# Kernel tuning notes

Hardware: AMD Instinct MI355X
Metric: run time of the kernel (lower is better)

Reference implementation:

```python
import jax, jax.numpy as jnp
import numpy as np

N_NODES = 100000
N_EDGES = 3200000
IN_FEAT = 256
OUT_FEAT = 128

def setup_inputs() -> dict:
    key = jax.random.key(0)
    k1, k2, k3, k4, k5 = jax.random.split(key, 5)
    feat = jax.random.normal(k1, (N_NODES, IN_FEAT), dtype=jnp.float32)
    edge_row = jnp.sort(jax.random.randint(k2, (N_EDGES,), 0, N_NODES, dtype=jnp.int32))
    edge_col = jax.random.randint(k3, (N_EDGES,), 0, N_NODES, dtype=jnp.int32)
    edge_val = jax.random.uniform(k4, (N_EDGES,), dtype=jnp.float32)
    # Xavier-uniform init like the torch module
    limit = float(np.sqrt(6.0 / (IN_FEAT + OUT_FEAT)))
    weight = jax.random.uniform(k5, (IN_FEAT, OUT_FEAT), dtype=jnp.float32, minval=-limit, maxval=limit)
    return {"feat": feat, "edge_row": edge_row, "edge_col": edge_col, "edge_val": edge_val, "weight": weight}

def reference(feat, edge_row, edge_col, edge_val, weight):
    # feat_embedding = feat @ W            [N, out_feat]
    feat_embedding = jnp.matmul(feat, weight)
    # x = spmm(adj, feat_embedding): out[i] = sum_{edges e: row[e]=i} val[e] * femb[col[e]]
    messages = edge_val[:, None] * feat_embedding[edge_col]  # [E, out_feat]
    x = jax.ops.segment_sum(messages, edge_row, num_segments=N_NODES)
    return (feat_embedding, x)
```

## Files before the change

kernel.cpp:

```cpp
#include <hip/hip_runtime.h>
#include <hip/hip_fp16.h>

#define IN_FEAT 256
#define OUT_FEAT 128

typedef _Float16 half8 __attribute__((ext_vector_type(8)));
typedef float    f32x4 __attribute__((ext_vector_type(4)));

#define GBM 128
#define GT  512

__global__ __launch_bounds__(GT, 1) void gemm_mfma_kernel(
    const float* __restrict__ A, const float* __restrict__ W,
    float* __restrict__ C, __half* __restrict__ Ch, int M, int writeHalf)
{
    __shared__ _Float16 sA[GBM * IN_FEAT];
    __shared__ _Float16 sW[OUT_FEAT * IN_FEAT];

    const int t    = threadIdx.x;
    const int row0 = blockIdx.x * GBM;

    {
        const int row = t >> 2;
        const int kq  = t & 3;
        int grow = row0 + row; if (grow >= M) grow = M - 1;
        const float* Ap = &A[(size_t)grow * IN_FEAT];
        #pragma unroll
        for (int i = 0; i < 8; ++i) {
            int k = kq * 8 + i * 32;
            float4 a0 = *(const float4*)(Ap + k);
            float4 a1 = *(const float4*)(Ap + k + 4);
            half8 h;
            h[0]=(_Float16)a0.x; h[1]=(_Float16)a0.y; h[2]=(_Float16)a0.z; h[3]=(_Float16)a0.w;
            h[4]=(_Float16)a1.x; h[5]=(_Float16)a1.y; h[6]=(_Float16)a1.z; h[7]=(_Float16)a1.w;
            int byte = row * 512 + k * 2;
            byte ^= (row & 7) << 4;
            *(half8*)((char*)sA + byte) = h;
        }
    }
    {
        const int col = t & 127;
        const int kq  = t >> 7;
        #pragma unroll
        for (int i = 0; i < 16; ++i) {
            int k = kq * 64 + i * 4;
            _Float16 h[4];
            h[0] = (_Float16)W[(size_t)(k+0) * OUT_FEAT + col];
            h[1] = (_Float16)W[(size_t)(k+1) * OUT_FEAT + col];
            h[2] = (_Float16)W[(size_t)(k+2) * OUT_FEAT + col];
            h[3] = (_Float16)W[(size_t)(k+3) * OUT_FEAT + col];
            int byte = col * 512 + k * 2;
            byte ^= (col & 7) << 4;
            *(unsigned long long*)((char*)sW + byte) = *(const unsigned long long*)h;
        }
    }
    __syncthreads();

    const int wid  = t >> 6;
    const int lane = t & 63;
    const int rowBase = wid * 16;
    const int fr = lane & 15;
    const int fk = lane >> 4;

    f32x4 acc[8];
    #pragma unroll
    for (int nt = 0; nt < 8; ++nt) acc[nt] = (f32x4){0.f, 0.f, 0.f, 0.f};

    #pragma unroll
    for (int ks = 0; ks < 8; ++ks) {
        const int arow  = rowBase + fr;
        int abyte = arow * 512 + ks * 64 + fk * 16;
        abyte ^= (arow & 7) << 4;
        half8 af = *(const half8*)((const char*)sA + abyte);
        #pragma unroll
        for (int nt = 0; nt < 8; ++nt) {
            const int col = nt * 16 + fr;
            int bbyte = col * 512 + ks * 64 + fk * 16;
            bbyte ^= (col & 7) << 4;
            half8 bf = *(const half8*)((const char*)sW + bbyte);
            acc[nt] = __builtin_amdgcn_mfma_f32_16x16x32_f16(af, bf, acc[nt], 0, 0, 0);
        }
    }

    const int drow = fk * 4;
    #pragma unroll
    for (int nt = 0; nt < 8; ++nt) {
        #pragma unroll
        for (int r = 0; r < 4; ++r) {
            int grow = row0 + rowBase + drow + r;
            if (grow < M) {
                int col = nt * 16 + fr;
                C[(size_t)grow * OUT_FEAT + col] = acc[nt][r];
                if (writeHalf)
                    *(_Float16*)&Ch[(size_t)grow * OUT_FEAT + col] = (_Float16)acc[nt][r];
            }
        }
    }
}

__global__ void zero_kernel(float4* __restrict__ p, int n4)
{
    int i      = blockIdx.x * blockDim.x + threadIdx.x;
    int stride = gridDim.x * blockDim.x;
    for (; i < n4; i += stride) p[i] = float4{0.f, 0.f, 0.f, 0.f};
}

#define EPB 512
#define EPW 128
#define PF  16

template<int USE_H>
__global__ __launch_bounds__(256) void spmm_kernel(
    const int*   __restrict__ erow, const int* __restrict__ ecol,
    const float* __restrict__ eval, const float* __restrict__ femb,
    const __half* __restrict__ fembh, float* __restrict__ x, int E)
{
    __shared__ int   s_row[EPB];
    __shared__ int   s_col[EPB];
    __shared__ float s_val[EPB];

    const int blockBase = blockIdx.x * EPB;

    #pragma unroll
    for (int i = 0; i < 2; ++i) {
        int li = threadIdx.x + i * 256;
        int e  = blockBase + li;
        if (e < E) {
            s_row[li] = __builtin_nontemporal_load(&erow[e]);
            s_col[li] = __builtin_nontemporal_load(&ecol[e]);
            s_val[li] = __builtin_nontemporal_load(&eval[e]);
        }
    }
    __syncthreads();

    const int wave = threadIdx.x >> 6;
    const int lane = threadIdx.x & 63;
    const int j    = lane * 2;

    const int w0 = wave * EPW;
    const int g0 = blockBase + w0;
    if (g0 >= E) return;
    const int n = min(EPW, E - g0);

    float2 acc = {0.f, 0.f};
    int cur = s_row[w0];

    if (n == EPW) {
        #pragma unroll 1
        for (int base = 0; base < EPW; base += PF) {
            __half2 h[PF];
            float2  f[PF];
            if constexpr (USE_H) {
                #pragma unroll
                for (int i = 0; i < PF; ++i) {
                    int c = s_col[w0 + base + i];
                    h[i] = *(const __half2*)&fembh[(size_t)c * OUT_FEAT + j];
                }
            } else {
                #pragma unroll
                for (int i = 0; i < PF; ++i) {
                    int c = s_col[w0 + base + i];
                    f[i] = *(const float2*)&femb[(size_t)c * OUT_FEAT + j];
                }
            }
            #pragma unroll
            for (int i = 0; i < PF; ++i) {
                int r = s_row[w0 + base + i];
                if (r != cur) {
                    atomicAdd(&x[(size_t)cur * OUT_FEAT + j],     acc.x);
                    atomicAdd(&x[(size_t)cur * OUT_FEAT + j + 1], acc.y);
                    acc.x = 0.f; acc.y = 0.f;
                    cur = r;
                }
                float v = s_val[w0 + base + i];
                float2 fv;
                if constexpr (USE_H) fv = __half22float2(h[i]); else fv = f[i];
                acc.x = fmaf(v, fv.x, acc.x);
                acc.y = fmaf(v, fv.y, acc.y);
            }
        }
    } else {
        for (int idx = 0; idx < n; ++idx) {
            int r = s_row[w0 + idx];
            if (r != cur) {
                atomicAdd(&x[(size_t)cur * OUT_FEAT + j],     acc.x);
                atomicAdd(&x[(size_t)cur * OUT_FEAT + j + 1], acc.y);
                acc.x = 0.f; acc.y = 0.f;
                cur = r;
            }
            int c = s_col[w0 + idx];
            float v = s_val[w0 + idx];
            float2 fv;
            if constexpr (USE_H) fv = __half22float2(*(const __half2*)&fembh[(size_t)c * OUT_FEAT + j]);
            else                 fv = *(const float2*)&femb[(size_t)c * OUT_FEAT + j];
            acc.x = fmaf(v, fv.x, acc.x);
            acc.y = fmaf(v, fv.y, acc.y);
        }
    }
    atomicAdd(&x[(size_t)cur * OUT_FEAT + j],     acc.x);
    atomicAdd(&x[(size_t)cur * OUT_FEAT + j + 1], acc.y);
}

extern "C" void kernel_launch(void* const* d_in, const int* in_sizes, int n_in,
                              void* d_out, int out_size, void* d_ws, size_t ws_size,
                              hipStream_t stream)
{
    const float* feat = (const float*)d_in[0];
    const int*   erow = (const int*)  d_in[1];
    const int*   ecol = (const int*)  d_in[2];
    const float* eval = (const float*)d_in[3];
    const float* W    = (const float*)d_in[4];

    const int M = in_sizes[0] / IN_FEAT;
    const int E = in_sizes[1];

    float*  femb  = (float*)d_out;
    float*  x     = femb + (size_t)M * OUT_FEAT;
    __half* fembh = (__half*)d_ws;

    const size_t needH = (size_t)M * OUT_FEAT * sizeof(__half);
    const int useH = (ws_size >= needH) ? 1 : 0;

    gemm_mfma_kernel<<<(M + GBM - 1) / GBM, GT, 0, stream>>>(feat, W, femb, fembh, M, useH);

    zero_kernel<<<2048, 256, 0, stream>>>((float4*)x, (M * OUT_FEAT) / 4);

    int nblk = (E + EPB - 1) / EPB;
    if (useH) spmm_kernel<1><<<nblk, 256, 0, stream>>>(erow, ecol, eval, femb, fembh, x, E);
    else      spmm_kernel<0><<<nblk, 256, 0, stream>>>(erow, ecol, eval, femb, fembh, x, E);
}
```

Baseline: 362.0 us.

## Precompute swizzled fp16 weight tile and vectorize GEMM output stores

Measured after the change: 359.5 us. No clear change (-0.7%).

```diff
diff --git a/kernel.cpp b/kernel.cpp
--- a/kernel.cpp
+++ b/kernel.cpp
@@ -5,13 +5,32 @@
 #define OUT_FEAT 128
 
 typedef _Float16 half8 __attribute__((ext_vector_type(8)));
+typedef _Float16 half4 __attribute__((ext_vector_type(4)));
 typedef float    f32x4 __attribute__((ext_vector_type(4)));
+
+#define WT_BYTES (OUT_FEAT * IN_FEAT * 2)
+
+__global__ __launch_bounds__(256) void wprep_kernel(
+    const float* __restrict__ W, char* __restrict__ wt)
+{
+    int t   = blockIdx.x * blockDim.x + threadIdx.x;
+    int col = t & 127;
+    int k   = (t >> 7) * 2;
+    _Float16 h0 = (_Float16)W[(size_t)k       * OUT_FEAT + col];
+    _Float16 h1 = (_Float16)W[(size_t)(k + 1) * OUT_FEAT + col];
+    int byte = col * 512 + k * 2;
+    byte ^= (col & 7) << 4;
+    unsigned short u0, u1;
+    __builtin_memcpy(&u0, &h0, 2);
+    __builtin_memcpy(&u1, &h1, 2);
+    *(unsigned int*)(wt + byte) = (unsigned int)u0 | ((unsigned int)u1 << 16);
+}
 
 #define GBM 128
 #define GT  512
 
 __global__ __launch_bounds__(GT, 1) void gemm_mfma_kernel(
-    const float* __restrict__ A, const float* __restrict__ W,
+    const float* __restrict__ A, const char* __restrict__ wt,
     float* __restrict__ C, __half* __restrict__ Ch, int M, int writeHalf)
 {
     __shared__ _Float16 sA[GBM * IN_FEAT];
@@ -39,20 +58,10 @@
         }
     }
     {
-        const int col = t & 127;
-        const int kq  = t >> 7;
-        #pragma unroll
-        for (int i = 0; i < 16; ++i) {
-            int k = kq * 64 + i * 4;
-            _Float16 h[4];
-            h[0] = (_Float16)W[(size_t)(k+0) * OUT_FEAT + col];
-            h[1] = (_Float16)W[(size_t)(k+1) * OUT_FEAT + col];
-            h[2] = (_Float16)W[(size_t)(k+2) * OUT_FEAT + col];
-            h[3] = (_Float16)W[(size_t)(k+3) * OUT_FEAT + col];
-            int byte = col * 512 + k * 2;
-            byte ^= (col & 7) << 4;
-            *(unsigned long long*)((char*)sW + byte) = *(const unsigned long long*)h;
-        }
+        const float4* src = (const float4*)wt;
+        float4*       dst = (float4*)sW;
+        #pragma unroll
+        for (int i = 0; i < 8; ++i) dst[t + GT * i] = src[t + GT * i];
     }
     __syncthreads();
 
@@ -78,21 +87,20 @@
             int bbyte = col * 512 + ks * 64 + fk * 16;
             bbyte ^= (col & 7) << 4;
             half8 bf = *(const half8*)((const char*)sW + bbyte);
-            acc[nt] = __builtin_amdgcn_mfma_f32_16x16x32_f16(af, bf, acc[nt], 0, 0, 0);
-        }
-    }
-
-    const int drow = fk * 4;
-    #pragma unroll
-    for (int nt = 0; nt < 8; ++nt) {
-        #pragma unroll
-        for (int r = 0; r < 4; ++r) {
-            int grow = row0 + rowBase + drow + r;
-            if (grow < M) {
-                int col = nt * 16 + fr;
-                C[(size_t)grow * OUT_FEAT + col] = acc[nt][r];
-                if (writeHalf)
-                    *(_Float16*)&Ch[(size_t)grow * OUT_FEAT + col] = (_Float16)acc[nt][r];
+            acc[nt] = __builtin_amdgcn_mfma_f32_16x16x32_f16(bf, af, acc[nt], 0, 0, 0);
+        }
+    }
+
+    const int grow = row0 + rowBase + fr;
+    if (grow < M) {
+        #pragma unroll
+        for (int nt = 0; nt < 8; ++nt) {
+            const int col0 = nt * 16 + fk * 4;
+            float4 o = {acc[nt][0], acc[nt][1], acc[nt][2], acc[nt][3]};
+            *(float4*)&C[(size_t)grow * OUT_FEAT + col0] = o;
+            if (writeHalf) {
+                half4 h = {(_Float16)o.x, (_Float16)o.y, (_Float16)o.z, (_Float16)o.w};
+                *(half4*)&Ch[(size_t)grow * OUT_FEAT + col0] = h;
             }
         }
     }
@@ -216,12 +224,15 @@
 
     float*  femb  = (float*)d_out;
     float*  x     = femb + (size_t)M * OUT_FEAT;
-    __half* fembh = (__half*)d_ws;
-
-    const size_t needH = (size_t)M * OUT_FEAT * sizeof(__half);
+    char*   wt    = (char*)d_ws;
+    __half* fembh = (__half*)((char*)d_ws + WT_BYTES);
+
+    const size_t needH = (size_t)WT_BYTES + (size_t)M * OUT_FEAT * sizeof(__half);
     const int useH = (ws_size >= needH) ? 1 : 0;
 
-    gemm_mfma_kernel<<<(M + GBM - 1) / GBM, GT, 0, stream>>>(feat, W, femb, fembh, M, useH);
+    wprep_kernel<<<64, 256, 0, stream>>>(W, wt);
+
+    gemm_mfma_kernel<<<(M + GBM - 1) / GBM, GT, 0, stream>>>(feat, wt, femb, fembh, M, useH);
 
     zero_kernel<<<2048, 256, 0, stream>>>((float4*)x, (M * OUT_FEAT) / 4);
 
```
